# Optimization experiments

Measured on AMD Instinct MI355X. Metric: run time of the kernel, lower is better.

Reference implementation:

```python
import jax, jax.numpy as jnp
from jax import lax
import numpy as np

D_MODEL = 64
D_STATE = 16
D_CONV = 4
EXPAND = 2
D_INNER = EXPAND * D_MODEL          # 128
DT_RANK = (D_MODEL + 15) // 16      # 4
B, H, W = 1, 256, 256
EPS = 1e-5


def _silu(v):
    return v * jax.nn.sigmoid(v)


def _mamba(seq, in_w, conv_w, conv_b, xproj_w, dt_w, dt_b, A_log, D, out_w):
    # seq: [b, L, d_model] -> [b, L, d_model]; official Mamba-1 block math.
    b, L, _ = seq.shape
    xz = seq @ in_w.T                              # [b,L,2*d_inner]
    x, z = jnp.split(xz, 2, axis=-1)
    # causal depthwise conv1d (kernel D_CONV), matches torch conv1d w/ left pad
    x_pad = jnp.pad(x, ((0, 0), (D_CONV - 1, 0), (0, 0)))
    x = sum(x_pad[:, k:k + L, :] * conv_w[:, k] for k in range(D_CONV)) + conv_b
    x = _silu(x)
    x_dbl = x @ xproj_w.T                          # [b,L,dt_rank+2*d_state]
    dt = jax.nn.softplus(x_dbl[..., :DT_RANK] @ dt_w.T + dt_b)   # [b,L,d_inner]
    Bm = x_dbl[..., DT_RANK:DT_RANK + D_STATE]     # [b,L,n]
    Cm = x_dbl[..., DT_RANK + D_STATE:]            # [b,L,n]
    A = -jnp.exp(A_log)                            # [d_inner,n]

    def step(h, inp):
        x_t, dt_t, B_t, C_t = inp                  # [b,d],[b,d],[b,n],[b,n]
        h = jnp.exp(dt_t[..., None] * A) * h + (dt_t * x_t)[..., None] * B_t[:, None, :]
        return h, jnp.einsum('bdn,bn->bd', h, C_t)

    h0 = jnp.zeros((b, D_INNER, D_STATE), seq.dtype)
    xs = tuple(jnp.swapaxes(t, 0, 1) for t in (x, dt, Bm, Cm))
    _, ys = lax.scan(step, h0, xs)                 # ys: [L,b,d_inner]
    y = jnp.swapaxes(ys, 0, 1) + x * D
    y = y * _silu(z)
    return y @ out_w.T


def _bidir(seq, params):
    fwd = _mamba(seq, *params)
    bwd = jnp.flip(_mamba(jnp.flip(seq, 1), *params), 1)
    return 0.5 * (fwd + bwd)


def setup_inputs() -> dict:
    key = jax.random.key(0)

    def mamba_params(k, prefix):
        ks = jax.random.split(k, 5)
        return {
            prefix + 'in_w': 0.05 * jax.random.normal(ks[0], (2 * D_INNER, D_MODEL), jnp.float32),
            prefix + 'conv_w': 0.2 * jax.random.normal(ks[1], (D_INNER, D_CONV), jnp.float32),
            prefix + 'conv_b': jnp.zeros((D_INNER,), jnp.float32),
            prefix + 'xproj_w': 0.05 * jax.random.normal(ks[2], (DT_RANK + 2 * D_STATE, D_INNER), jnp.float32),
            prefix + 'dt_w': 0.1 * jax.random.normal(ks[3], (D_INNER, DT_RANK), jnp.float32),
            prefix + 'dt_b': jnp.full((D_INNER,), float(np.log(np.expm1(0.02))), jnp.float32),
            prefix + 'A_log': jnp.log(jnp.tile(jnp.arange(1, D_STATE + 1, dtype=jnp.float32), (D_INNER, 1))),
            prefix + 'D': jnp.ones((D_INNER,), jnp.float32),
            prefix + 'out_w': 0.05 * jax.random.normal(ks[4], (D_MODEL, D_INNER), jnp.float32),
        }

    k1, k2, k3, k4 = jax.random.split(key, 4)
    inp = {
        'x': jax.random.normal(k1, (B, D_MODEL, H, W), jnp.float32),
        'gn_w': jnp.ones((D_MODEL,), jnp.float32),
        'gn_b': jnp.zeros((D_MODEL,), jnp.float32),
        'proj_w': 0.02 * jax.random.normal(k4, (D_MODEL, D_MODEL), jnp.float32),
    }
    inp.update(mamba_params(k2, 'row_'))
    inp.update(mamba_params(k3, 'col_'))
    return inp


def reference(x, gn_w, gn_b,
              row_in_w, row_conv_w, row_conv_b, row_xproj_w, row_dt_w, row_dt_b, row_A_log, row_D, row_out_w,
              col_in_w, col_conv_w, col_conv_b, col_xproj_w, col_dt_w, col_dt_b, col_A_log, col_D, col_out_w,
              proj_w):
    residual = x
    # GroupNorm(1, dim): normalize over (C,H,W) per sample, per-channel affine
    mean = jnp.mean(x, axis=(1, 2, 3), keepdims=True)
    var = jnp.mean((x - mean) ** 2, axis=(1, 2, 3), keepdims=True)
    y = (x - mean) * lax.rsqrt(var + EPS) * gn_w[None, :, None, None] + gn_b[None, :, None, None]
    b, c, h, w = y.shape
    row_p = (row_in_w, row_conv_w, row_conv_b, row_xproj_w, row_dt_w, row_dt_b, row_A_log, row_D, row_out_w)
    col_p = (col_in_w, col_conv_w, col_conv_b, col_xproj_w, col_dt_w, col_dt_b, col_A_log, col_D, col_out_w)
    rows = y.transpose(0, 2, 3, 1).reshape(b * h, w, c)            # scan along W
    row_y = _bidir(rows, row_p).reshape(b, h, w, c).transpose(0, 3, 1, 2)
    cols = y.transpose(0, 3, 2, 1).reshape(b * w, h, c)            # scan along H
    col_y = _bidir(cols, col_p).reshape(b, w, h, c).transpose(0, 3, 2, 1)
    y = 0.5 * (row_y + col_y)
    y = jnp.einsum('oc,bchw->bohw', proj_w, y)                     # 1x1 conv, no bias
    return residual + y
```

## Files before the change

### kernel.cpp

```cpp
#include <hip/hip_runtime.h>


static constexpr size_t OFF_YN   = 0;
static constexpr size_t OFF_XZ   = OFF_YN + 4194304;
static constexpr size_t OFF_ACCD = OFF_XZ + 16777216;
static constexpr size_t WS_FLOATS = OFF_ACCD + 16777216;

__device__ __forceinline__ float silu_f(float v) { return v / (1.f + __expf(-v)); }

__global__ void k_zero(float* r) {
    if (threadIdx.x < 2) r[threadIdx.x] = 0.f;
}

__global__ __launch_bounds__(256) void k_reduce(const float* __restrict__ x, float* __restrict__ red) {
    int tid = blockIdx.x * 256 + threadIdx.x;
    const float4* x4 = (const float4*)x;
    float s = 0.f, sq = 0.f;
    #pragma unroll
    for (int i = 0; i < 4; i++) {
        float4 v = x4[tid + i * 262144];
        s  += v.x + v.y + v.z + v.w;
        sq += v.x * v.x + v.y * v.y + v.z * v.z + v.w * v.w;
    }
    #pragma unroll
    for (int off = 32; off; off >>= 1) {
        s  += __shfl_down(s, off);
        sq += __shfl_down(sq, off);
    }
    __shared__ float ls[8], lq[8];
    int wid = threadIdx.x >> 6, lane = threadIdx.x & 63;
    if (lane == 0) { ls[wid] = s; lq[wid] = sq; }
    __syncthreads();
    if (threadIdx.x == 0) {
        float ts = 0.f, tq = 0.f;
        for (int w = 0; w < 4; w++) { ts += ls[w]; tq += lq[w]; }
        atomicAdd(&red[0], ts);
        atomicAdd(&red[1], tq);
    }
}

__global__ __launch_bounds__(256) void k_norm(const float* __restrict__ x, const float* __restrict__ red,
                                              const float* __restrict__ gw, const float* __restrict__ gb,
                                              float* __restrict__ yn) {
    __shared__ float tile[64][65];
    int hw0 = blockIdx.x * 64;
    float mean = red[0] * (1.f / 4194304.f);
    float var  = red[1] * (1.f / 4194304.f) - mean * mean;
    float rstd = rsqrtf(var + 1e-5f);
    int tx = threadIdx.x & 63, ty = threadIdx.x >> 6;
    #pragma unroll
    for (int i = 0; i < 16; i++) {
        int c = i * 4 + ty;
        tile[c][tx] = x[c * 65536 + hw0 + tx];
    }
    __syncthreads();
    int c = tx;
    float sc = gw[c] * rstd;
    float bb = gb[c] - mean * sc;
    #pragma unroll
    for (int i = 0; i < 16; i++) {
        int m = i * 4 + ty;
        yn[(size_t)(hw0 + m) * 64 + c] = tile[c][m] * sc + bb;
    }
}

__global__ __launch_bounds__(256) void k_xz(const float* __restrict__ yn, const float* __restrict__ in_w,
                                            float* __restrict__ xz, int orient) {
    __shared__ __align__(16) float tk[64][68];
    __shared__ __align__(16) float wl[64][132];
    int mt = blockIdx.x >> 1, nc = blockIdx.x & 1;
    int t0 = mt * 64;
    int tid = threadIdx.x;
    {
        int k = tid & 63, mg = tid >> 6;
        for (int ms = 0; ms < 64; ms += 4) {
            int m = ms + mg;
            int t = t0 + m;
            size_t addr;
            if (orient == 0) addr = (size_t)t * 64 + k;
            else { int s = t >> 8, p = t & 255; addr = (size_t)(p * 256 + s) * 64 + k; }
            tk[k][m] = yn[addr];
        }
    }
    {
        int k = tid & 63, ng = tid >> 6;
        for (int i = 0; i < 32; i++) {
            int n = i * 4 + ng;
            wl[k][n] = in_w[(size_t)(nc * 128 + n) * 64 + k];
        }
    }
    __syncthreads();
    int m0 = (tid & 15) * 4, n0 = (tid >> 4) * 8;
    float acc[4][8];
    #pragma unroll
    for (int i = 0; i < 4; i++)
        #pragma unroll
        for (int j = 0; j < 8; j++) acc[i][j] = 0.f;
    #pragma unroll 4
    for (int k = 0; k < 64; k++) {
        float4 tv = *(const float4*)&tk[k][m0];
        float tvf[4] = { tv.x, tv.y, tv.z, tv.w };
        #pragma unroll
        for (int i4 = 0; i4 < 2; i4++) {
            float4 wv = *(const float4*)&wl[k][n0 + i4 * 4];
            float wvf[4] = { wv.x, wv.y, wv.z, wv.w };
            #pragma unroll
            for (int m = 0; m < 4; m++)
                #pragma unroll
                for (int j = 0; j < 4; j++)
                    acc[m][i4 * 4 + j] += tvf[m] * wvf[j];
        }
    }
    #pragma unroll
    for (int m = 0; m < 4; m++) {
        size_t t = t0 + m0 + m;
        #pragma unroll
        for (int i4 = 0; i4 < 2; i4++) {
            float4 v = { acc[m][i4 * 4 + 0], acc[m][i4 * 4 + 1], acc[m][i4 * 4 + 2], acc[m][i4 * 4 + 3] };
            *(float4*)&xz[t * 256 + nc * 128 + n0 + i4 * 4] = v;
        }
    }
}

__global__ __launch_bounds__(512) void k_fused(const float* __restrict__ xz,
                                               const float* __restrict__ conv_w, const float* __restrict__ conv_b,
                                               const float* __restrict__ xproj_w,
                                               const float* __restrict__ dt_w, const float* __restrict__ dt_b,
                                               const float* __restrict__ A_log, const float* __restrict__ Dw,
                                               const float* __restrict__ out_w,
                                               float* __restrict__ accD) {
    __shared__ __align__(16) float sm[16272];
    float* xw = sm;
    float* wp = sm + 8960;
    float* xd = sm + 8960 + 4752;
    const int tid = threadIdx.x;
    const int s = blockIdx.x, dir = blockIdx.y;
    const int seqbase = s * 256;

    for (int i = 0; i < 10; i++) {
        int lin = i * 512 + tid;
        if (lin < 4608) {
            int n = lin >> 7, k = lin & 127;
            wp[n * 132 + k] = xproj_w[lin];
        }
    }

    const int d  = tid >> 2, q = tid & 3, q4 = q * 4;
    const int dg = tid & 127;
    const int mg = tid >> 7;
    const float4 cw  = ((const float4*)conv_w)[dg];
    const float  cb  = conv_b[dg];
    const float4 dwv = ((const float4*)dt_w)[d];
    const float  dbv = dt_b[d];
    const float A0 = -__expf(A_log[d * 16 + q4 + 0]);
    const float A1 = -__expf(A_log[d * 16 + q4 + 1]);
    const float A2 = -__expf(A_log[d * 16 + q4 + 2]);
    const float A3 = -__expf(A_log[d * 16 + q4 + 3]);
    const float Dv = Dw[d];
    float* ap = accD + (size_t)dir * 4194304 + (size_t)seqbase * 64;

    float h0 = 0.f, h1 = 0.f, h2 = 0.f, h3 = 0.f;

    for (int ci = 0; ci < 4; ci++) {
        const int c  = dir ? 3 - ci : ci;
        const int p0 = c * 64;
        __syncthreads();
        for (int i = 0; i < 18; i++) {
            int lin = i * 512 + tid;
            if (lin < 8960) {
                int pi = lin >> 7, dd = lin & 127;
                int pp = p0 - 3 + pi;
                float v = 0.f;
                if (pp >= 0 && pp < 256) v = xz[(size_t)(seqbase + pp) * 256 + dd];
                xw[lin] = v;
            }
        }
        __syncthreads();
        float cv[16];
        #pragma unroll
        for (int i = 0; i < 16; i++) {
            int m = i * 4 + mg;
            float v;
            if (dir == 0)
                v = cw.x * xw[m * 128 + dg] + cw.y * xw[(m + 1) * 128 + dg] +
                    cw.z * xw[(m + 2) * 128 + dg] + cw.w * xw[(m + 3) * 128 + dg];
            else
                v = cw.x * xw[(m + 6) * 128 + dg] + cw.y * xw[(m + 5) * 128 + dg] +
                    cw.z * xw[(m + 4) * 128 + dg] + cw.w * xw[(m + 3) * 128 + dg];
            v += cb;
            cv[i] = silu_f(v);
        }
        __syncthreads();
        #pragma unroll
        for (int i = 0; i < 16; i++) {
            int m = i * 4 + mg;
            xw[m * 132 + dg] = cv[i];
        }
        __syncthreads();
        {
            const int m = tid >> 3, g = tid & 7;
            float acc5[5] = { 0.f, 0.f, 0.f, 0.f, 0.f };
            for (int k4 = 0; k4 < 32; k4++) {
                float4 xv = *(const float4*)&xw[m * 132 + k4 * 4];
                #pragma unroll
                for (int j = 0; j < 5; j++) {
                    int n = g + 8 * j;
                    if (n < 36) {
                        float4 wv = *(const float4*)&wp[n * 132 + k4 * 4];
                        acc5[j] += xv.x * wv.x + xv.y * wv.y + xv.z * wv.z + xv.w * wv.w;
                    }
                }
            }
            #pragma unroll
            for (int j = 0; j < 5; j++) {
                int n = g + 8 * j;
                if (n < 36) xd[m * 40 + n] = acc5[j];
            }
        }
        __syncthreads();
        {
            int t = dir ? 63 : 0;
            const int tstep = dir ? -1 : 1;
            float4 r = *(const float4*)&xd[t * 40];
            float dt_n = dbv + r.x * dwv.x + r.y * dwv.y + r.z * dwv.z + r.w * dwv.w;
            dt_n = (dt_n > 20.f) ? dt_n : log1pf(__expf(dt_n));
            float  xv_n = xw[t * 132 + d];
            float4 B4_n = *(const float4*)&xd[t * 40 + 4 + q4];
            float4 C4_n = *(const float4*)&xd[t * 40 + 20 + q4];
            float e0_n = __expf(dt_n * A0), e1_n = __expf(dt_n * A1);
            float e2_n = __expf(dt_n * A2), e3_n = __expf(dt_n * A3);
            for (int step = 0; step < 64; step++) {
                const int tw = t;
                const float dtv = dt_n, xv = xv_n;
                const float4 B4 = B4_n, C4 = C4_n;
                const float e0 = e0_n, e1 = e1_n, e2 = e2_n, e3 = e3_n;
                if (step < 63) {
                    t += tstep;
                    float4 rn = *(const float4*)&xd[t * 40];
                    dt_n = dbv + rn.x * dwv.x + rn.y * dwv.y + rn.z * dwv.z + rn.w * dwv.w;
                    dt_n = (dt_n > 20.f) ? dt_n : log1pf(__expf(dt_n));
                    xv_n = xw[t * 132 + d];
                    B4_n = *(const float4*)&xd[t * 40 + 4 + q4];
                    C4_n = *(const float4*)&xd[t * 40 + 20 + q4];
                    e0_n = __expf(dt_n * A0); e1_n = __expf(dt_n * A1);
                    e2_n = __expf(dt_n * A2); e3_n = __expf(dt_n * A3);
                }
                const float dx = dtv * xv;
                h0 = e0 * h0 + dx * B4.x;
                h1 = e1 * h1 + dx * B4.y;
                h2 = e2 * h2 + dx * B4.z;
                h3 = e3 * h3 + dx * B4.w;
                float y = h0 * C4.x + h1 * C4.y + h2 * C4.z + h3 * C4.w;
                y += __shfl_xor(y, 1);
                y += __shfl_xor(y, 2);
                if (q == 0) xw[tw * 132 + d] = y + xv * Dv;
            }
        }
        __syncthreads();
        #pragma unroll
        for (int i = 0; i < 16; i++) {
            int m = i * 4 + mg;
            float yc = xw[m * 132 + dg];
            float zv = xz[(size_t)(seqbase + p0 + m) * 256 + 128 + dg];
            xw[m * 132 + dg] = yc * silu_f(zv);
        }
        __syncthreads();
        {
            const int m = tid >> 3, n0 = (tid & 7) * 8;
            float a8[8] = { 0.f, 0.f, 0.f, 0.f, 0.f, 0.f, 0.f, 0.f };
            for (int k4 = 0; k4 < 32; k4++) {
                float4 xv = *(const float4*)&xw[m * 132 + k4 * 4];
                #pragma unroll
                for (int nn = 0; nn < 8; nn++) {
                    float4 wv = *(const float4*)&out_w[(n0 + nn) * 128 + k4 * 4];
                    a8[nn] += xv.x * wv.x + xv.y * wv.y + xv.z * wv.z + xv.w * wv.w;
                }
            }
            float4 v0 = { a8[0], a8[1], a8[2], a8[3] };
            float4 v1 = { a8[4], a8[5], a8[6], a8[7] };
            *(float4*)&ap[(size_t)(p0 + m) * 64 + n0]     = v0;
            *(float4*)&ap[(size_t)(p0 + m) * 64 + n0 + 4] = v1;
        }
    }
}

__global__ __launch_bounds__(256) void k_final(const float* __restrict__ accD,
                                               const float* __restrict__ pw, const float* __restrict__ x,
                                               float* __restrict__ out) {
    __shared__ __align__(16) float tk[64][68];
    __shared__ __align__(16) float wl[64][68];
    int t0 = blockIdx.x * 64, tid = threadIdx.x;
    int hh = t0 >> 8, w0 = t0 & 255;
    for (int i = 0; i < 16; i++) {
        int m = i * 4 + (tid >> 6), k = tid & 63;
        size_t rt = (size_t)(t0 + m) * 64 + k;
        size_t ct = (size_t)((w0 + m) * 256 + hh) * 64 + k;
        tk[k][m] = 0.25f * (accD[rt] + accD[4194304 + rt] +
                            accD[8388608 + ct] + accD[12582912 + ct]);
    }
    for (int i = 0; i < 16; i++) {
        int n = i * 4 + (tid >> 6), k = tid & 63;
        wl[k][n] = pw[n * 64 + k];
    }
    __syncthreads();
    int m0 = (tid & 15) * 4, n0 = (tid >> 4) * 4;
    float a4[4][4];
    #pragma unroll
    for (int i = 0; i < 4; i++)
        #pragma unroll
        for (int j = 0; j < 4; j++) a4[i][j] = 0.f;
    #pragma unroll 4
    for (int k = 0; k < 64; k++) {
        float4 tv = *(const float4*)&tk[k][m0];
        float4 wv = *(const float4*)&wl[k][n0];
        float tvf[4] = { tv.x, tv.y, tv.z, tv.w };
        float wvf[4] = { wv.x, wv.y, wv.z, wv.w };
        #pragma unroll
        for (int m = 0; m < 4; m++)
            #pragma unroll
            for (int j = 0; j < 4; j++)
                a4[m][j] += tvf[m] * wvf[j];
    }
    #pragma unroll
    for (int j = 0; j < 4; j++) {
        int n = n0 + j;
        float4 r = *(const float4*)&x[(size_t)n * 65536 + t0 + m0];
        float4 v = { a4[0][j] + r.x, a4[1][j] + r.y, a4[2][j] + r.z, a4[3][j] + r.w };
        *(float4*)&out[(size_t)n * 65536 + t0 + m0] = v;
    }
}

extern "C" void kernel_launch(void* const* d_in, const int* in_sizes, int n_in,
                              void* d_out, int out_size, void* d_ws, size_t ws_size,
                              hipStream_t stream) {
    (void)n_in; (void)out_size;
    if (ws_size < WS_FLOATS * sizeof(float)) return;

    float* ws = (float*)d_ws;
    const float* x    = (const float*)d_in[0];
    const float* gn_w = (const float*)d_in[1];
    const float* gn_b = (const float*)d_in[2];

    int rbase, cbase;
    const float* proj_w;
    if (in_sizes[3] == 64 * 64) { proj_w = (const float*)d_in[3]; rbase = 4; cbase = 13; }
    else                        { rbase = 3; cbase = 12; proj_w = (const float*)d_in[21]; }

    float* yn   = ws + OFF_YN;
    float* xzb  = ws + OFF_XZ;
    float* accD = ws + OFF_ACCD;
    float* red  = ws + OFF_ACCD;

    k_zero<<<1, 64, 0, stream>>>(red);
    k_reduce<<<1024, 256, 0, stream>>>(x, red);
    k_norm<<<1024, 256, 0, stream>>>(x, red, gn_w, gn_b, yn);

    for (int o = 0; o < 2; o++) {
        int base = (o == 0) ? rbase : cbase;
        const float* in_w    = (const float*)d_in[base + 0];
        const float* conv_w  = (const float*)d_in[base + 1];
        const float* conv_b  = (const float*)d_in[base + 2];
        const float* xproj_w = (const float*)d_in[base + 3];
        const float* dt_w    = (const float*)d_in[base + 4];
        const float* dt_b    = (const float*)d_in[base + 5];
        const float* A_log   = (const float*)d_in[base + 6];
        const float* Dp      = (const float*)d_in[base + 7];
        const float* out_w   = (const float*)d_in[base + 8];

        k_xz<<<2048, 256, 0, stream>>>(yn, in_w, xzb, o);
        k_fused<<<dim3(256, 2), 512, 0, stream>>>(xzb, conv_w, conv_b, xproj_w,
                                                  dt_w, dt_b, A_log, Dp, out_w,
                                                  accD + (size_t)o * 8388608);
    }

    k_final<<<1024, 256, 0, stream>>>(accD, proj_w, x, (float*)d_out);
}
```

Before: 1.977 ms.

## Halve chunk size in fused Mamba kernel to cut shared memory and raise occupancy

Processes each sequence in 8 chunks of 32 positions instead of 4 chunks of 64, which shrinks the shared buffer from about 65KB to about 41KB, and sets a launch-bounds minimum of 6 blocks. The conv1d now reads x straight from global memory into registers with a sliding window instead of staging a halo tile in LDS. The x-projection and out-projection thread mappings are remapped to fit the smaller tile, and the scan drops its software-prefetched next-step values in favour of a plain loop using fast log. More resident blocks should hide latency better, at the cost of twice as many barrier phases and possible register spilling under the tighter occupancy bound.

```diff
diff --git a/kernel.cpp b/kernel.cpp
--- a/kernel.cpp
+++ b/kernel.cpp
@@ -122,27 +122,25 @@
     }
 }
 
-__global__ __launch_bounds__(512) void k_fused(const float* __restrict__ xz,
+__global__ __launch_bounds__(512, 6) void k_fused(const float* __restrict__ xz,
                                                const float* __restrict__ conv_w, const float* __restrict__ conv_b,
                                                const float* __restrict__ xproj_w,
                                                const float* __restrict__ dt_w, const float* __restrict__ dt_b,
                                                const float* __restrict__ A_log, const float* __restrict__ Dw,
                                                const float* __restrict__ out_w,
                                                float* __restrict__ accD) {
-    __shared__ __align__(16) float sm[16272];
-    float* xw = sm;
-    float* wp = sm + 8960;
-    float* xd = sm + 8960 + 4752;
+    __shared__ __align__(16) float sm[10256];
+    float* xcl = sm;
+    float* wp  = sm + 4224;
+    float* xd  = sm + 4224 + 4752;
     const int tid = threadIdx.x;
     const int s = blockIdx.x, dir = blockIdx.y;
     const int seqbase = s * 256;
 
-    for (int i = 0; i < 10; i++) {
+    #pragma unroll
+    for (int i = 0; i < 9; i++) {
         int lin = i * 512 + tid;
-        if (lin < 4608) {
-            int n = lin >> 7, k = lin & 127;
-            wp[n * 132 + k] = xproj_w[lin];
-        }
+        wp[(lin >> 7) * 132 + (lin & 127)] = xproj_w[lin];
     }
 
     const int d  = tid >> 2, q = tid & 3, q4 = q * 4;
@@ -157,95 +155,63 @@
     const float A2 = -__expf(A_log[d * 16 + q4 + 2]);
     const float A3 = -__expf(A_log[d * 16 + q4 + 3]);
     const float Dv = Dw[d];
+    const float w0 = dir ? cw.w : cw.x, w1 = dir ? cw.z : cw.y;
+    const float w2 = dir ? cw.y : cw.z, w3 = dir ? cw.x : cw.w;
     float* ap = accD + (size_t)dir * 4194304 + (size_t)seqbase * 64;
 
     float h0 = 0.f, h1 = 0.f, h2 = 0.f, h3 = 0.f;
 
-    for (int ci = 0; ci < 4; ci++) {
-        const int c  = dir ? 3 - ci : ci;
-        const int p0 = c * 64;
-        __syncthreads();
-        for (int i = 0; i < 18; i++) {
-            int lin = i * 512 + tid;
-            if (lin < 8960) {
-                int pi = lin >> 7, dd = lin & 127;
-                int pp = p0 - 3 + pi;
-                float v = 0.f;
-                if (pp >= 0 && pp < 256) v = xz[(size_t)(seqbase + pp) * 256 + dd];
-                xw[lin] = v;
-            }
-        }
-        __syncthreads();
-        float cv[16];
-        #pragma unroll
-        for (int i = 0; i < 16; i++) {
-            int m = i * 4 + mg;
-            float v;
-            if (dir == 0)
-                v = cw.x * xw[m * 128 + dg] + cw.y * xw[(m + 1) * 128 + dg] +
-                    cw.z * xw[(m + 2) * 128 + dg] + cw.w * xw[(m + 3) * 128 + dg];
-            else
-                v = cw.x * xw[(m + 6) * 128 + dg] + cw.y * xw[(m + 5) * 128 + dg] +
-                    cw.z * xw[(m + 4) * 128 + dg] + cw.w * xw[(m + 3) * 128 + dg];
-            v += cb;
-            cv[i] = silu_f(v);
-        }
-        __syncthreads();
-        #pragma unroll
-        for (int i = 0; i < 16; i++) {
-            int m = i * 4 + mg;
-            xw[m * 132 + dg] = cv[i];
-        }
+    for (int hci = 0; hci < 8; hci++) {
+        const int hc = dir ? 7 - hci : hci;
+        const int p0 = hc * 32;
         __syncthreads();
         {
-            const int m = tid >> 3, g = tid & 7;
-            float acc5[5] = { 0.f, 0.f, 0.f, 0.f, 0.f };
+            const int lbase = p0 + mg * 8 + (dir ? 0 : -3);
+            float a[11];
+            #pragma unroll
+            for (int j = 0; j < 11; j++) {
+                int lp = lbase + j;
+                a[j] = (lp >= 0 && lp < 256) ? xz[(size_t)(seqbase + lp) * 256 + dg] : 0.f;
+            }
+            #pragma unroll
+            for (int j = 0; j < 8; j++) {
+                float v = w0 * a[j] + w1 * a[j + 1] + w2 * a[j + 2] + w3 * a[j + 3] + cb;
+                xcl[(mg * 8 + j) * 132 + dg] = silu_f(v);
+            }
+        }
+        __syncthreads();
+        {
+            const int lm = tid >> 4, g = tid & 15;
+            float ac0 = 0.f, ac1 = 0.f, ac2 = 0.f;
             for (int k4 = 0; k4 < 32; k4++) {
-                float4 xv = *(const float4*)&xw[m * 132 + k4 * 4];
-                #pragma unroll
-                for (int j = 0; j < 5; j++) {
-                    int n = g + 8 * j;
-                    if (n < 36) {
-                        float4 wv = *(const float4*)&wp[n * 132 + k4 * 4];
-                        acc5[j] += xv.x * wv.x + xv.y * wv.y + xv.z * wv.z + xv.w * wv.w;
-                    }
+                float4 xv = *(const float4*)&xcl[lm * 132 + k4 * 4];
+                float4 wa = *(const float4*)&wp[g * 132 + k4 * 4];
+                float4 wb = *(const float4*)&wp[(g + 16) * 132 + k4 * 4];
+                ac0 += xv.x * wa.x + xv.y * wa.y + xv.z * wa.z + xv.w * wa.w;
+                ac1 += xv.x * wb.x + xv.y * wb.y + xv.z * wb.z + xv.w * wb.w;
+                if (g < 4) {
+                    float4 wc = *(const float4*)&wp[(g + 32) * 132 + k4 * 4];
+                    ac2 += xv.x * wc.x + xv.y * wc.y + xv.z * wc.z + xv.w * wc.w;
                 }
             }
-            #pragma unroll
-            for (int j = 0; j < 5; j++) {
-                int n = g + 8 * j;
-                if (n < 36) xd[m * 40 + n] = acc5[j];
-            }
+            xd[lm * 40 + g]      = ac0;
+            xd[lm * 40 + 16 + g] = ac1;
+            if (g < 4) xd[lm * 40 + 32 + g] = ac2;
         }
         __syncthreads();
         {
-            int t = dir ? 63 : 0;
+            int t = dir ? 31 : 0;
             const int tstep = dir ? -1 : 1;
-            float4 r = *(const float4*)&xd[t * 40];
-            float dt_n = dbv + r.x * dwv.x + r.y * dwv.y + r.z * dwv.z + r.w * dwv.w;
-            dt_n = (dt_n > 20.f) ? dt_n : log1pf(__expf(dt_n));
-            float  xv_n = xw[t * 132 + d];
-            float4 B4_n = *(const float4*)&xd[t * 40 + 4 + q4];
-            float4 C4_n = *(const float4*)&xd[t * 40 + 20 + q4];
-            float e0_n = __expf(dt_n * A0), e1_n = __expf(dt_n * A1);
-            float e2_n = __expf(dt_n * A2), e3_n = __expf(dt_n * A3);
-            for (int step = 0; step < 64; step++) {
-                const int tw = t;
-                const float dtv = dt_n, xv = xv_n;
-                const float4 B4 = B4_n, C4 = C4_n;
-                const float e0 = e0_n, e1 = e1_n, e2 = e2_n, e3 = e3_n;
-                if (step < 63) {
-                    t += tstep;
-                    float4 rn = *(const float4*)&xd[t * 40];
-                    dt_n = dbv + rn.x * dwv.x + rn.y * dwv.y + rn.z * dwv.z + rn.w * dwv.w;
-                    dt_n = (dt_n > 20.f) ? dt_n : log1pf(__expf(dt_n));
-                    xv_n = xw[t * 132 + d];
-                    B4_n = *(const float4*)&xd[t * 40 + 4 + q4];
-                    C4_n = *(const float4*)&xd[t * 40 + 20 + q4];
-                    e0_n = __expf(dt_n * A0); e1_n = __expf(dt_n * A1);
-                    e2_n = __expf(dt_n * A2); e3_n = __expf(dt_n * A3);
-                }
-                const float dx = dtv * xv;
+            for (int step = 0; step < 32; step++) {
+                float4 r = *(const float4*)&xd[t * 40];
+                float dtv = dbv + r.x * dwv.x + r.y * dwv.y + r.z * dwv.z + r.w * dwv.w;
+                dtv = (dtv > 20.f) ? dtv : __logf(1.f + __expf(dtv));
+                float xv = xcl[t * 132 + d];
+                float4 B4 = *(const float4*)&xd[t * 40 + 4 + q4];
+                float4 C4 = *(const float4*)&xd[t * 40 + 20 + q4];
+                float e0 = __expf(dtv * A0), e1 = __expf(dtv * A1);
+                float e2 = __expf(dtv * A2), e3 = __expf(dtv * A3);
+                float dx = dtv * xv;
                 h0 = e0 * h0 + dx * B4.x;
                 h1 = e1 * h1 + dx * B4.y;
                 h2 = e2 * h2 + dx * B4.z;
@@ -253,33 +219,36 @@
                 float y = h0 * C4.x + h1 * C4.y + h2 * C4.z + h3 * C4.w;
                 y += __shfl_xor(y, 1);
                 y += __shfl_xor(y, 2);
-                if (q == 0) xw[tw * 132 + d] = y + xv * Dv;
-            }
-        }
-        __syncthreads();
-        #pragma unroll
-        for (int i = 0; i < 16; i++) {
-            int m = i * 4 + mg;
-            float yc = xw[m * 132 + dg];
-            float zv = xz[(size_t)(seqbase + p0 + m) * 256 + 128 + dg];
-            xw[m * 132 + dg] = yc * silu_f(zv);
+                if (q == 0) xcl[t * 132 + d] = y + xv * Dv;
+                t += tstep;
+            }
+        }
+        __syncthreads();
+        #pragma unroll
+        for (int j = 0; j < 8; j++) {
+            int lm = mg * 8 + j;
+            float yc = xcl[lm * 132 + dg];
+            float zv = xz[(size_t)(seqbase + p0 + lm) * 256 + 128 + dg];
+            xcl[lm * 132 + dg] = yc * silu_f(zv);
         }
         __syncthreads();
         {
-            const int m = tid >> 3, n0 = (tid & 7) * 8;
-            float a8[8] = { 0.f, 0.f, 0.f, 0.f, 0.f, 0.f, 0.f, 0.f };
+            const int rep = tid >> 8, m = (tid >> 3) & 31;
+            const int n0 = rep * 32 + (tid & 7) * 4;
+            float a0 = 0.f, a1 = 0.f, a2 = 0.f, a3 = 0.f;
             for (int k4 = 0; k4 < 32; k4++) {
-                float4 xv = *(const float4*)&xw[m * 132 + k4 * 4];
-                #pragma unroll
-                for (int nn = 0; nn < 8; nn++) {
-                    float4 wv = *(const float4*)&out_w[(n0 + nn) * 128 + k4 * 4];
-                    a8[nn] += xv.x * wv.x + xv.y * wv.y + xv.z * wv.z + xv.w * wv.w;
-                }
-            }
-            float4 v0 = { a8[0], a8[1], a8[2], a8[3] };
-            float4 v1 = { a8[4], a8[5], a8[6], a8[7] };
-            *(float4*)&ap[(size_t)(p0 + m) * 64 + n0]     = v0;
-            *(float4*)&ap[(size_t)(p0 + m) * 64 + n0 + 4] = v1;
+                float4 xv = *(const float4*)&xcl[m * 132 + k4 * 4];
+                float4 v0 = *(const float4*)&out_w[(n0 + 0) * 128 + k4 * 4];
+                float4 v1 = *(const float4*)&out_w[(n0 + 1) * 128 + k4 * 4];
+                float4 v2 = *(const float4*)&out_w[(n0 + 2) * 128 + k4 * 4];
+                float4 v3 = *(const float4*)&out_w[(n0 + 3) * 128 + k4 * 4];
+                a0 += xv.x * v0.x + xv.y * v0.y + xv.z * v0.z + xv.w * v0.w;
+                a1 += xv.x * v1.x + xv.y * v1.y + xv.z * v1.z + xv.w * v1.w;
+                a2 += xv.x * v2.x + xv.y * v2.y + xv.z * v2.z + xv.w * v2.w;
+                a3 += xv.x * v3.x + xv.y * v3.y + xv.z * v3.z + xv.w * v3.w;
+            }
+            float4 v = { a0, a1, a2, a3 };
+            *(float4*)&ap[(size_t)(p0 + m) * 64 + n0] = v;
         }
     }
 }
```

After: 6.398 ms. 3.24x slower.
